# Performance work log

Hardware: AMD Instinct MI355X
Metric: run time of the kernel (lower is better)

Reference implementation:

```python
import jax, jax.numpy as jnp
import numpy as np

B, N, D = 4, 2048, 1024
DF = 4 * D
EPS = 1e-5


def _layernorm(x, w, b):
    mu = jnp.mean(x, axis=-1, keepdims=True)
    var = jnp.mean(jnp.square(x - mu), axis=-1, keepdims=True)
    return (x - mu) * jax.lax.rsqrt(var + EPS) * w + b


def setup_inputs() -> dict:
    key = jax.random.key(0)
    ks = jax.random.split(key, 8)
    x = jax.random.normal(ks[0], (B, N, D), dtype=jnp.float32)
    # conv filter param (torch init is zeros; use small randn for numeric coverage)
    weights = jax.random.normal(ks[1], (1, 1, N), dtype=jnp.float32) * 0.02
    # registered buffer: sqrt(1/(i+1)) per token, shape (1, N, 1)
    scale = jnp.sqrt(1.0 / (jnp.arange(N, dtype=jnp.float32) + 1.0))[None, :, None]
    ln1_w = jnp.ones((D,), jnp.float32)
    ln1_b = jnp.zeros((D,), jnp.float32)
    W1 = jax.random.normal(ks[2], (DF, D), dtype=jnp.float32) * 0.02
    b1 = jnp.zeros((DF,), jnp.float32)
    W2 = jax.random.normal(ks[3], (D, DF), dtype=jnp.float32) * 0.02
    b2 = jnp.zeros((D,), jnp.float32)
    scalar = jax.random.normal(ks[4], (1,), dtype=jnp.float32) * 0.1
    ln2_w = jnp.ones((D,), jnp.float32)
    ln2_b = jnp.zeros((D,), jnp.float32)
    return dict(x=x, weights=weights, scale=scale, ln1_w=ln1_w, ln1_b=ln1_b,
                W1=W1, b1=b1, W2=W2, b2=b2, scalar=scalar, ln2_w=ln2_w, ln2_b=ln2_b)


def reference(x, weights, scale, ln1_w, ln1_b, W1, b1, W2, b2, scalar, ln2_w, ln2_b):
    n = weights.shape[-1]
    # FFT token-mixing conv: operate over token axis. x: (B,N,D) -> (B,D,N)
    xt = jnp.swapaxes(x, -2, -1)
    # real inputs -> rfft/irfft equals real(ifft(fft*fft)) from the torch code
    prod = jnp.fft.rfft(xt, n=2 * n) * jnp.fft.rfft(weights, n=2 * n)
    conv = jnp.fft.irfft(prod, n=2 * n)[..., :n]  # (B,D,N)
    x1 = jnp.swapaxes(conv, -2, -1)               # (B,N,D)
    x1 = _layernorm(x + x1 * scale, ln1_w, ln1_b)
    # GELU MLP (torch F.gelu default = exact erf gelu)
    h = jax.nn.gelu(jnp.einsum('bnd,fd->bnf', x1, W1) + b1, approximate=False)
    mlp = jnp.einsum('bnf,df->bnd', h, W2) + b2
    x2 = _layernorm(x1 + scalar * mlp, ln2_w, ln2_b)
    return x2
```

## Files before the change

kernel.cpp:

```cpp
#include <hip/hip_runtime.h>
#include <cstdint>

typedef float floatx4 __attribute__((ext_vector_type(4)));
typedef float floatx16 __attribute__((ext_vector_type(16)));
typedef int intx8 __attribute__((ext_vector_type(8)));

__device__ __forceinline__ unsigned short f2b(float f) {
  union { float f; unsigned u; } v; v.f = f;
  return (unsigned short)((v.u + 0x7FFFu + ((v.u >> 16) & 1u)) >> 16);
}
__device__ __forceinline__ float b2f(unsigned short h) {
  union { unsigned u; float f; } v; v.u = ((unsigned)h) << 16;
  return v.f;
}

__device__ __forceinline__ void gload_lds16(const void* g, void* l) {
  __builtin_amdgcn_global_load_lds(
      (const __attribute__((address_space(1))) void*)g,
      (__attribute__((address_space(3))) void*)l, 16, 0, 0);
}

__device__ __forceinline__ intx8 lds_read32(const unsigned char* p) {
  union { intx8 v; int4 q[2]; } u;
  u.q[0] = *(const int4*)p;
  u.q[1] = *(const int4*)(p + 16);
  return u.v;
}

__device__ __forceinline__ int swz_scol(int lane) {
  const int q = (lane >> 1) & 3;
  const int r3 = (lane >> 3) & 3;
  const int sbit = lane & 1;
  return ((((q ^ r3) << 1) | sbit) << 4);
}


__global__ void cast_f8x64_kernel(const float* __restrict__ in,
                                  int* __restrict__ out) {
  long i = (long)blockIdx.x * 256 + threadIdx.x;
  float4 v = ((const float4*)in)[i];
  int pk = __builtin_amdgcn_cvt_pk_fp8_f32(v.x * 64.0f, v.y * 64.0f, 0, false);
  pk = __builtin_amdgcn_cvt_pk_fp8_f32(v.z * 64.0f, v.w * 64.0f, pk, true);
  out[i] = pk;
}

__global__ void build_T8_kernel(const float* __restrict__ w,
                                int* __restrict__ T8) {
  long i = (long)blockIdx.x * 256 + threadIdx.x;
  int n = (int)(i >> 9);
  int m0 = (int)(i & 511) * 4;
  float v[4];
#pragma unroll
  for (int r = 0; r < 4; ++r) {
    int m = m0 + r;
    v[r] = (m <= n) ? w[n - m] * 64.0f : 0.0f;
  }
  int pk = __builtin_amdgcn_cvt_pk_fp8_f32(v[0], v[1], 0, false);
  pk = __builtin_amdgcn_cvt_pk_fp8_f32(v[2], v[3], pk, true);
  T8[i] = pk;
}

__global__ void transpose_cast_f8_kernel(const float* __restrict__ x,
                                         unsigned char* __restrict__ xT) {
  __shared__ float tile[32][33];
  int b = blockIdx.z;
  int n0 = blockIdx.y * 32;
  int d0 = blockIdx.x * 32;
  int tx = threadIdx.x;
  int ty = threadIdx.y;
  for (int i = ty; i < 32; i += 8)
    tile[i][tx] = x[((long)b * 2048 + n0 + i) * 1024 + d0 + tx];
  __syncthreads();
  float a = tile[ty * 4 + 0][tx];
  float c = tile[ty * 4 + 1][tx];
  float e = tile[ty * 4 + 2][tx];
  float f = tile[ty * 4 + 3][tx];
  int pk = __builtin_amdgcn_cvt_pk_fp8_f32(a, c, 0, false);
  pk = __builtin_amdgcn_cvt_pk_fp8_f32(e, f, pk, true);
  *(int*)(xT + ((long)b * 1024 + d0 + tx) * 2048 + n0 + ty * 4) = pk;
}

template <int EPI, int NT, bool TRI>
__global__ __launch_bounds__(256, 4) void gemm_f8(
    const unsigned char* __restrict__ A, const unsigned char* __restrict__ B,
    int Kstride, int Kloop, long zsA, long zsB, long zsC,
    int rx, int ryb, int gxn, unsigned sclA, unsigned sclB,
    const float* __restrict__ resid, const float* __restrict__ scale,
    const float* __restrict__ bias,
    float* __restrict__ Cf, unsigned short* __restrict__ Cb,
    unsigned char* __restrict__ C8) {
  __shared__ __align__(16) unsigned char As[16 * 1040];
  __shared__ __align__(16) unsigned char Bs[16 * 1040];
  const int tid = threadIdx.x;
  const int wid = tid >> 6;
  const int lane = tid & 63;
  const int l32 = lane & 31;
  const int half = lane >> 5;
  const int wm = (wid >> 1) * 64;
  const int wn = (wid & 1) * 64;

  const int bid = blockIdx.x;
  const int xcd = bid & 7;
  const int ib = bid >> 3;
  const int ci = ib % rx;
  const int ri = ib / rx;
  long bm, bn;
  if (TRI) {
    bm = (long)(ri == 0 ? xcd : 15 - xcd) * 128;
    bn = (long)ci * 128;
  } else {
    const int gx = xcd % gxn;
    const int gy = xcd / gxn;
    bm = (long)(gy * ryb + ri) * 128;
    bn = (long)(gx * rx + ci) * 128;
  }
  const int bz = blockIdx.z;
  const unsigned char* Ab = A + zsA * bz;
  const unsigned char* Bb = B + zsB * bz;

  floatx16 acc[2][2];
#pragma unroll
  for (int i = 0; i < 2; ++i)
#pragma unroll
    for (int j = 0; j < 2; ++j)
#pragma unroll
      for (int e = 0; e < 16; ++e) acc[i][j][e] = 0.0f;

  const int srow = tid >> 3;
  const int scol = swz_scol(lane);
  const unsigned char* gA[4];
  const unsigned char* gB[4];
  unsigned char* lA[4];
  unsigned char* lB[4];
#pragma unroll
  for (int p = 0; p < 4; ++p) {
    gA[p] = Ab + (bm + p * 32 + srow) * (long)Kstride + scol;
    gB[p] = Bb + (bn + p * 32 + srow) * (long)Kstride + scol;
    lA[p] = As + (p * 4 + wid) * 1040;
    lB[p] = Bs + (p * 4 + wid) * 1040;
  }

  int offA[2][2], offB[2][2];
#pragma unroll
  for (int i = 0; i < 2; ++i)
#pragma unroll
    for (int s = 0; s < 2; ++s) {
      const int ra = wm + i * 32 + l32;
      const int ca = (s * 2 + half) ^ (ra & 3);
      offA[i][s] = (ra >> 3) * 1040 + (ra & 7) * 128 + (ca << 5);
      const int rb = wn + i * 32 + l32;
      const int cb = (s * 2 + half) ^ (rb & 3);
      offB[i][s] = (rb >> 3) * 1040 + (rb & 7) * 128 + (cb << 5);
    }

  const int kend = TRI ? min(Kloop, (int)bm + 128) : Kloop;
  for (int kk = 0; kk < kend; kk += 128) {
    __syncthreads();
#pragma unroll
    for (int p = 0; p < 4; ++p) {
      gload_lds16(gA[p] + kk, lA[p]);
      gload_lds16(gB[p] + kk, lB[p]);
    }
    __syncthreads();
#pragma unroll
    for (int s = 0; s < 2; ++s) {
      intx8 b0 = lds_read32(Bs + offB[0][s]);
      intx8 b1 = lds_read32(Bs + offB[1][s]);
      intx8 a0 = lds_read32(As + offA[0][s]);
      intx8 a1 = lds_read32(As + offA[1][s]);
      acc[0][0] = __builtin_amdgcn_mfma_scale_f32_32x32x64_f8f6f4(
          a0, b0, acc[0][0], 0, 0, 0, sclA, 0, sclB);
      acc[0][1] = __builtin_amdgcn_mfma_scale_f32_32x32x64_f8f6f4(
          a0, b1, acc[0][1], 0, 0, 0, sclA, 0, sclB);
      acc[1][0] = __builtin_amdgcn_mfma_scale_f32_32x32x64_f8f6f4(
          a1, b0, acc[1][0], 0, 0, 0, sclA, 0, sclB);
      acc[1][1] = __builtin_amdgcn_mfma_scale_f32_32x32x64_f8f6f4(
          a1, b1, acc[1][1], 0, 0, 0, sclA, 0, sclB);
    }
  }

#pragma unroll
  for (int i = 0; i < 2; ++i)
#pragma unroll
    for (int j = 0; j < 2; ++j)
#pragma unroll
      for (int r = 0; r < 16; ++r) {
        long row = bm + wm + i * 32 + (r & 3) + 8 * (r >> 2) + 4 * half;
        long col = bn + wn + j * 32 + l32;
        long idx = (long)bz * zsC + row * (long)NT + col;
        float v = acc[i][j][r];
        if (EPI == 0) {
          Cb[idx] = f2b(v);
        } else if (EPI == 1) {
          Cf[idx] = resid[idx] + scale[row] * v;
        } else {
          v += bias[col];
          float u = v * (0.7978845608f + 0.0356774081f * v * v);
          float u2 = u * u;
          float t = __fdividef(u * (15.0f + u2), 15.0f + 6.0f * u2);
          t = fminf(fmaxf(t, -1.0f), 1.0f);
          float g = 0.5f * v * (1.0f + t);
          int pk = __builtin_amdgcn_cvt_pk_fp8_f32(g, 0.0f, 0, false);
          C8[idx] = (unsigned char)(pk & 0xFF);
        }
      }
}

__global__ __launch_bounds__(256) void ln_kernel(
    const float* __restrict__ in, const float* __restrict__ w,
    const float* __restrict__ b, unsigned short* __restrict__ outb,
    int* __restrict__ outf8) {
  const long row = blockIdx.x;
  const int tid = threadIdx.x;
  float4 v = ((const float4*)in)[row * 256 + tid];
  float s = v.x + v.y + v.z + v.w;
  float ss = v.x * v.x + v.y * v.y + v.z * v.z + v.w * v.w;
#pragma unroll
  for (int off = 32; off > 0; off >>= 1) {
    s += __shfl_down(s, off);
    ss += __shfl_down(ss, off);
  }
  __shared__ float red[8];
  const int wid = tid >> 6, lane = tid & 63;
  if (lane == 0) { red[wid] = s; red[4 + wid] = ss; }
  __syncthreads();
  s = red[0] + red[1] + red[2] + red[3];
  ss = red[4] + red[5] + red[6] + red[7];
  const float mu = s * (1.0f / 1024.0f);
  const float var = ss * (1.0f / 1024.0f) - mu * mu;
  const float rs = rsqrtf(var + 1e-5f);
  float4 wv = ((const float4*)w)[tid];
  float4 bv = ((const float4*)b)[tid];
  float o0 = (v.x - mu) * rs * wv.x + bv.x;
  float o1 = (v.y - mu) * rs * wv.y + bv.y;
  float o2 = (v.z - mu) * rs * wv.z + bv.z;
  float o3 = (v.w - mu) * rs * wv.w + bv.w;
  ushort4 u{f2b(o0), f2b(o1), f2b(o2), f2b(o3)};
  ((ushort4*)outb)[row * 256 + tid] = u;
  int pk = __builtin_amdgcn_cvt_pk_fp8_f32(o0, o1, 0, false);
  pk = __builtin_amdgcn_cvt_pk_fp8_f32(o2, o3, pk, true);
  outf8[row * 256 + tid] = pk;
}

__global__ __launch_bounds__(256) void ln2_fused_kernel(
    const unsigned short* __restrict__ y0, const unsigned short* __restrict__ y1,
    const unsigned short* __restrict__ x1b, const float* __restrict__ b2,
    const float* __restrict__ scalar_p, const float* __restrict__ w,
    const float* __restrict__ b, float* __restrict__ out) {
  const long row = blockIdx.x;
  const int tid = threadIdx.x;
  ushort4 a4 = ((const ushort4*)y0)[row * 256 + tid];
  ushort4 c4 = ((const ushort4*)y1)[row * 256 + tid];
  ushort4 xr = ((const ushort4*)x1b)[row * 256 + tid];
  float4 bias = ((const float4*)b2)[tid];
  const float scl = scalar_p[0];
  float4 v;
  v.x = b2f(xr.x) + scl * (b2f(a4.x) + b2f(c4.x) + bias.x);
  v.y = b2f(xr.y) + scl * (b2f(a4.y) + b2f(c4.y) + bias.y);
  v.z = b2f(xr.z) + scl * (b2f(a4.z) + b2f(c4.z) + bias.z);
  v.w = b2f(xr.w) + scl * (b2f(a4.w) + b2f(c4.w) + bias.w);
  float s = v.x + v.y + v.z + v.w;
  float ss = v.x * v.x + v.y * v.y + v.z * v.z + v.w * v.w;
#pragma unroll
  for (int off = 32; off > 0; off >>= 1) {
    s += __shfl_down(s, off);
    ss += __shfl_down(ss, off);
  }
  __shared__ float red[8];
  const int wid = tid >> 6, lane = tid & 63;
  if (lane == 0) { red[wid] = s; red[4 + wid] = ss; }
  __syncthreads();
  s = red[0] + red[1] + red[2] + red[3];
  ss = red[4] + red[5] + red[6] + red[7];
  const float mu = s * (1.0f / 1024.0f);
  const float var = ss * (1.0f / 1024.0f) - mu * mu;
  const float rs = rsqrtf(var + 1e-5f);
  float4 wv = ((const float4*)w)[tid];
  float4 bv = ((const float4*)b)[tid];
  float4 o;
  o.x = (v.x - mu) * rs * wv.x + bv.x;
  o.y = (v.y - mu) * rs * wv.y + bv.y;
  o.z = (v.z - mu) * rs * wv.z + bv.z;
  o.w = (v.w - mu) * rs * wv.w + bv.w;
  ((float4*)out)[row * 256 + tid] = o;
}

extern "C" void kernel_launch(void* const* d_in, const int* in_sizes, int n_in,
                              void* d_out, int out_size, void* d_ws, size_t ws_size,
                              hipStream_t stream) {
  const float* x      = (const float*)d_in[0];
  const float* wconv  = (const float*)d_in[1];
  const float* scale  = (const float*)d_in[2];
  const float* ln1w   = (const float*)d_in[3];
  const float* ln1b   = (const float*)d_in[4];
  const float* W1     = (const float*)d_in[5];
  const float* b1     = (const float*)d_in[6];
  const float* W2     = (const float*)d_in[7];
  const float* b2     = (const float*)d_in[8];
  const float* scalar = (const float*)d_in[9];
  const float* ln2w   = (const float*)d_in[10];
  const float* ln2b   = (const float*)d_in[11];
  float* out = (float*)d_out;

  const unsigned SCL_1  = 0x7F7F7F7Fu;
  const unsigned SCL_64 = 0x79797979u;

  char* ws = (char*)d_ws;
  unsigned char* xT8   = (unsigned char*)ws;  ws += (size_t)4 * 1024 * 2048;
  unsigned char* T8    = (unsigned char*)ws;  ws += (size_t)2048 * 2048;
  unsigned char* W1f8  = (unsigned char*)ws;  ws += (size_t)4096 * 1024;
  unsigned char* W2f8  = (unsigned char*)ws;  ws += (size_t)4096 * 1024;
  float* y             = (float*)ws;          ws += (size_t)8192 * 1024 * 4;
  unsigned short* yb   = (unsigned short*)ws; ws += (size_t)2 * 8192 * 1024 * 2;
  unsigned short* x1b  = (unsigned short*)ws; ws += (size_t)8192 * 1024 * 2;
  unsigned char* x1f8  = (unsigned char*)ws;  ws += (size_t)8192 * 1024;
  unsigned char* h8    = (unsigned char*)ws;  ws += (size_t)8192 * 4096;

  cast_f8x64_kernel<<<4096, 256, 0, stream>>>(W1, (int*)W1f8);
  cast_f8x64_kernel<<<4096, 256, 0, stream>>>(W2, (int*)W2f8);
  build_T8_kernel<<<4096, 256, 0, stream>>>(wconv, (int*)T8);
  transpose_cast_f8_kernel<<<dim3(32, 64, 4), dim3(32, 8), 0, stream>>>(x, xT8);

  gemm_f8<1, 1024, true><<<dim3(128, 1, 4), 256, 0, stream>>>(
      T8, xT8, 2048, 2048, 0L, (long)1024 * 2048, (long)2048 * 1024,
      8, 0, 0, SCL_64, SCL_1, x, scale, nullptr, y, nullptr, nullptr);
  ln_kernel<<<8192, 256, 0, stream>>>(y, ln1w, ln1b, x1b, (int*)x1f8);
  gemm_f8<2, 4096, false><<<dim3(2048, 1, 1), 256, 0, stream>>>(
      x1f8, W1f8, 1024, 1024, 0L, 0L, 0L,
      16, 16, 2, SCL_1, SCL_64, nullptr, nullptr, b1, nullptr, nullptr, h8);
  gemm_f8<0, 1024, false><<<dim3(512, 1, 2), 256, 0, stream>>>(
      h8, W2f8, 4096, 2048, 2048L, 2048L, (long)8192 * 1024,
      8, 8, 1, SCL_1, SCL_64, nullptr, nullptr, nullptr, nullptr, yb, nullptr);
  ln2_fused_kernel<<<8192, 256, 0, stream>>>(
      yb, yb + (size_t)8192 * 1024, x1b, b2, scalar, ln2w, ln2b, out);
}
```

Before: 298.8 us.

## Split triangular conv GEMM along K, fuse prep kernels, widen LDS swizzle

The four preprocessing kernels (weight casts, Toeplitz build, transpose-cast of x) are merged into one launch. The causal Toeplitz conv GEMM is split in two along K to balance the triangular workload, doubling the grid. Each half writes bf16 partials, and the residual-plus-scale combine moves into a new LN1 kernel that reads both halves. The LDS swizzle is widened from 4 to 8 column groups to reduce bank conflicts, at the cost of extra partial-sum traffic and bf16 rounding of the conv output.

```diff
diff --git a/kernel.cpp b/kernel.cpp
--- a/kernel.cpp
+++ b/kernel.cpp
@@ -20,75 +20,74 @@
       (__attribute__((address_space(3))) void*)l, 16, 0, 0);
 }
 
-__device__ __forceinline__ intx8 lds_read32(const unsigned char* p) {
+__device__ __forceinline__ intx8 lds_read32s(const unsigned char* base,
+                                             int lo, int hi) {
   union { intx8 v; int4 q[2]; } u;
-  u.q[0] = *(const int4*)p;
-  u.q[1] = *(const int4*)(p + 16);
+  u.q[0] = *(const int4*)(base + lo);
+  u.q[1] = *(const int4*)(base + hi);
   return u.v;
 }
 
 __device__ __forceinline__ int swz_scol(int lane) {
-  const int q = (lane >> 1) & 3;
-  const int r3 = (lane >> 3) & 3;
-  const int sbit = lane & 1;
-  return ((((q ^ r3) << 1) | sbit) << 4);
-}
-
-
-__global__ void cast_f8x64_kernel(const float* __restrict__ in,
-                                  int* __restrict__ out) {
-  long i = (long)blockIdx.x * 256 + threadIdx.x;
-  float4 v = ((const float4*)in)[i];
-  int pk = __builtin_amdgcn_cvt_pk_fp8_f32(v.x * 64.0f, v.y * 64.0f, 0, false);
-  pk = __builtin_amdgcn_cvt_pk_fp8_f32(v.z * 64.0f, v.w * 64.0f, pk, true);
-  out[i] = pk;
-}
-
-__global__ void build_T8_kernel(const float* __restrict__ w,
-                                int* __restrict__ T8) {
-  long i = (long)blockIdx.x * 256 + threadIdx.x;
-  int n = (int)(i >> 9);
-  int m0 = (int)(i & 511) * 4;
-  float v[4];
-#pragma unroll
-  for (int r = 0; r < 4; ++r) {
-    int m = m0 + r;
-    v[r] = (m <= n) ? w[n - m] * 64.0f : 0.0f;
-  }
-  int pk = __builtin_amdgcn_cvt_pk_fp8_f32(v[0], v[1], 0, false);
-  pk = __builtin_amdgcn_cvt_pk_fp8_f32(v[2], v[3], pk, true);
-  T8[i] = pk;
-}
-
-__global__ void transpose_cast_f8_kernel(const float* __restrict__ x,
-                                         unsigned char* __restrict__ xT) {
-  __shared__ float tile[32][33];
-  int b = blockIdx.z;
-  int n0 = blockIdx.y * 32;
-  int d0 = blockIdx.x * 32;
-  int tx = threadIdx.x;
-  int ty = threadIdx.y;
-  for (int i = ty; i < 32; i += 8)
-    tile[i][tx] = x[((long)b * 2048 + n0 + i) * 1024 + d0 + tx];
-  __syncthreads();
-  float a = tile[ty * 4 + 0][tx];
-  float c = tile[ty * 4 + 1][tx];
-  float e = tile[ty * 4 + 2][tx];
-  float f = tile[ty * 4 + 3][tx];
-  int pk = __builtin_amdgcn_cvt_pk_fp8_f32(a, c, 0, false);
-  pk = __builtin_amdgcn_cvt_pk_fp8_f32(e, f, pk, true);
-  *(int*)(xT + ((long)b * 1024 + d0 + tx) * 2048 + n0 + ty * 4) = pk;
+  return (((lane & 7) ^ ((lane >> 3) & 7)) << 4);
+}
+
+__global__ __launch_bounds__(256) void prep_kernel(
+    const float* __restrict__ W1, const float* __restrict__ W2,
+    const float* __restrict__ wconv, const float* __restrict__ x,
+    int* __restrict__ W1f8, int* __restrict__ W2f8,
+    int* __restrict__ T8, unsigned char* __restrict__ xT) {
+  const int bid = blockIdx.x;
+  const int tid = threadIdx.x;
+  if (bid < 8192) {
+    const float* in = (bid < 4096) ? W1 : W2;
+    int* out = (bid < 4096) ? W1f8 : W2f8;
+    long i = (long)(bid & 4095) * 256 + tid;
+    float4 v = ((const float4*)in)[i];
+    int pk = __builtin_amdgcn_cvt_pk_fp8_f32(v.x * 64.0f, v.y * 64.0f, 0, false);
+    pk = __builtin_amdgcn_cvt_pk_fp8_f32(v.z * 64.0f, v.w * 64.0f, pk, true);
+    out[i] = pk;
+  } else if (bid < 12288) {
+    long i = (long)(bid - 8192) * 256 + tid;
+    int n = (int)(i >> 9);
+    int m0 = (int)(i & 511) * 4;
+    float v[4];
+#pragma unroll
+    for (int r = 0; r < 4; ++r) {
+      int m = m0 + r;
+      v[r] = (m <= n) ? wconv[n - m] * 64.0f : 0.0f;
+    }
+    int pk = __builtin_amdgcn_cvt_pk_fp8_f32(v[0], v[1], 0, false);
+    pk = __builtin_amdgcn_cvt_pk_fp8_f32(v[2], v[3], pk, true);
+    T8[i] = pk;
+  } else {
+    __shared__ float tile[32][33];
+    const int t = bid - 12288;
+    const int d0 = (t & 31) * 32;
+    const int n0 = ((t >> 5) & 63) * 32;
+    const int b = t >> 11;
+    const int tx = tid & 31;
+    const int ty = tid >> 5;
+    for (int i = ty; i < 32; i += 8)
+      tile[i][tx] = x[((long)b * 2048 + n0 + i) * 1024 + d0 + tx];
+    __syncthreads();
+    float a = tile[ty * 4 + 0][tx];
+    float c = tile[ty * 4 + 1][tx];
+    float e = tile[ty * 4 + 2][tx];
+    float f = tile[ty * 4 + 3][tx];
+    int pk = __builtin_amdgcn_cvt_pk_fp8_f32(a, c, 0, false);
+    pk = __builtin_amdgcn_cvt_pk_fp8_f32(e, f, pk, true);
+    *(int*)(xT + ((long)b * 1024 + d0 + tx) * 2048 + n0 + ty * 4) = pk;
+  }
 }
 
 template <int EPI, int NT, bool TRI>
 __global__ __launch_bounds__(256, 4) void gemm_f8(
     const unsigned char* __restrict__ A, const unsigned char* __restrict__ B,
-    int Kstride, int Kloop, long zsA, long zsB, long zsC,
+    int Kstride, int Kloop, long zsA, long zsB, long zsC, long zsP,
     int rx, int ryb, int gxn, unsigned sclA, unsigned sclB,
-    const float* __restrict__ resid, const float* __restrict__ scale,
     const float* __restrict__ bias,
-    float* __restrict__ Cf, unsigned short* __restrict__ Cb,
-    unsigned char* __restrict__ C8) {
+    unsigned short* __restrict__ Cb, unsigned char* __restrict__ C8) {
   __shared__ __align__(16) unsigned char As[16 * 1040];
   __shared__ __align__(16) unsigned char Bs[16 * 1040];
   const int tid = threadIdx.x;
@@ -102,17 +101,29 @@
   const int bid = blockIdx.x;
   const int xcd = bid & 7;
   const int ib = bid >> 3;
-  const int ci = ib % rx;
-  const int ri = ib / rx;
   long bm, bn;
+  int kstart, kend;
+  long pofs = 0;
   if (TRI) {
+    const int ci = ib & 7;
+    const int ri = (ib >> 3) & 1;
+    const int sp = ib >> 4;
     bm = (long)(ri == 0 ? xcd : 15 - xcd) * 128;
     bn = (long)ci * 128;
+    const int T = (int)(bm >> 7) + 1;
+    const int h = (T + 1) >> 1;
+    kstart = (sp ? h : 0) * 128;
+    kend = (sp ? T : h) * 128;
+    pofs = (long)sp * zsP;
   } else {
+    const int ci = ib % rx;
+    const int ri = ib / rx;
     const int gx = xcd % gxn;
     const int gy = xcd / gxn;
     bm = (long)(gy * ryb + ri) * 128;
     bn = (long)(gx * rx + ci) * 128;
+    kstart = 0;
+    kend = Kloop;
   }
   const int bz = blockIdx.z;
   const unsigned char* Ab = A + zsA * bz;
@@ -140,21 +151,23 @@
     lB[p] = Bs + (p * 4 + wid) * 1040;
   }
 
-  int offA[2][2], offB[2][2];
+  int offA_lo[2][2], offA_hi[2][2], offB_lo[2][2], offB_hi[2][2];
 #pragma unroll
   for (int i = 0; i < 2; ++i)
 #pragma unroll
     for (int s = 0; s < 2; ++s) {
-      const int ra = wm + i * 32 + l32;
-      const int ca = (s * 2 + half) ^ (ra & 3);
-      offA[i][s] = (ra >> 3) * 1040 + (ra & 7) * 128 + (ca << 5);
-      const int rb = wn + i * 32 + l32;
-      const int cb = (s * 2 + half) ^ (rb & 3);
-      offB[i][s] = (rb >> 3) * 1040 + (rb & 7) * 128 + (cb << 5);
+      const int q0 = s * 4 + half * 2;
+      const int ra = (int)wm + i * 32 + l32;
+      const int baseA = (ra >> 3) * 1040 + (ra & 7) * 128;
+      offA_lo[i][s] = baseA + ((q0 ^ (ra & 7)) << 4);
+      offA_hi[i][s] = baseA + (((q0 + 1) ^ (ra & 7)) << 4);
+      const int rb = (int)wn + i * 32 + l32;
+      const int baseB = (rb >> 3) * 1040 + (rb & 7) * 128;
+      offB_lo[i][s] = baseB + ((q0 ^ (rb & 7)) << 4);
+      offB_hi[i][s] = baseB + (((q0 + 1) ^ (rb & 7)) << 4);
     }
 
-  const int kend = TRI ? min(Kloop, (int)bm + 128) : Kloop;
-  for (int kk = 0; kk < kend; kk += 128) {
+  for (int kk = kstart; kk < kend; kk += 128) {
     __syncthreads();
 #pragma unroll
     for (int p = 0; p < 4; ++p) {
@@ -164,10 +177,10 @@
     __syncthreads();
 #pragma unroll
     for (int s = 0; s < 2; ++s) {
-      intx8 b0 = lds_read32(Bs + offB[0][s]);
-      intx8 b1 = lds_read32(Bs + offB[1][s]);
-      intx8 a0 = lds_read32(As + offA[0][s]);
-      intx8 a1 = lds_read32(As + offA[1][s]);
+      intx8 b0 = lds_read32s(Bs, offB_lo[0][s], offB_hi[0][s]);
+      intx8 b1 = lds_read32s(Bs, offB_lo[1][s], offB_hi[1][s]);
+      intx8 a0 = lds_read32s(As, offA_lo[0][s], offA_hi[0][s]);
+      intx8 a1 = lds_read32s(As, offA_lo[1][s], offA_hi[1][s]);
       acc[0][0] = __builtin_amdgcn_mfma_scale_f32_32x32x64_f8f6f4(
           a0, b0, acc[0][0], 0, 0, 0, sclA, 0, sclB);
       acc[0][1] = __builtin_amdgcn_mfma_scale_f32_32x32x64_f8f6f4(
@@ -187,12 +200,10 @@
       for (int r = 0; r < 16; ++r) {
         long row = bm + wm + i * 32 + (r & 3) + 8 * (r >> 2) + 4 * half;
         long col = bn + wn + j * 32 + l32;
-        long idx = (long)bz * zsC + row * (long)NT + col;
+        long idx = pofs + (long)bz * zsC + row * (long)NT + col;
         float v = acc[i][j][r];
         if (EPI == 0) {
           Cb[idx] = f2b(v);
-        } else if (EPI == 1) {
-          Cf[idx] = resid[idx] + scale[row] * v;
         } else {
           v += bias[col];
           float u = v * (0.7978845608f + 0.0356774081f * v * v);
@@ -206,13 +217,22 @@
       }
 }
 
-__global__ __launch_bounds__(256) void ln_kernel(
-    const float* __restrict__ in, const float* __restrict__ w,
-    const float* __restrict__ b, unsigned short* __restrict__ outb,
-    int* __restrict__ outf8) {
+__global__ __launch_bounds__(256) void ln1_kernel(
+    const float* __restrict__ x, const unsigned short* __restrict__ c0,
+    const unsigned short* __restrict__ c1, const float* __restrict__ scale,
+    const float* __restrict__ w, const float* __restrict__ b,
+    unsigned short* __restrict__ outb, int* __restrict__ outf8) {
   const long row = blockIdx.x;
   const int tid = threadIdx.x;
-  float4 v = ((const float4*)in)[row * 256 + tid];
+  float4 xv = ((const float4*)x)[row * 256 + tid];
+  ushort4 a4 = ((const ushort4*)c0)[row * 256 + tid];
+  ushort4 e4 = ((const ushort4*)c1)[row * 256 + tid];
+  const float sc = scale[row & 2047];
+  float4 v;
+  v.x = xv.x + sc * (b2f(a4.x) + b2f(e4.x));
+  v.y = xv.y + sc * (b2f(a4.y) + b2f(e4.y));
+  v.z = xv.z + sc * (b2f(a4.z) + b2f(e4.z));
+  v.w = xv.w + sc * (b2f(a4.w) + b2f(e4.w));
   float s = v.x + v.y + v.z + v.w;
   float ss = v.x * v.x + v.y * v.y + v.z * v.z + v.w * v.w;
 #pragma unroll
@@ -315,22 +335,22 @@
   unsigned short* x1b  = (unsigned short*)ws; ws += (size_t)8192 * 1024 * 2;
   unsigned char* x1f8  = (unsigned char*)ws;  ws += (size_t)8192 * 1024;
   unsigned char* h8    = (unsigned char*)ws;  ws += (size_t)8192 * 4096;
-
-  cast_f8x64_kernel<<<4096, 256, 0, stream>>>(W1, (int*)W1f8);
-  cast_f8x64_kernel<<<4096, 256, 0, stream>>>(W2, (int*)W2f8);
-  build_T8_kernel<<<4096, 256, 0, stream>>>(wconv, (int*)T8);
-  transpose_cast_f8_kernel<<<dim3(32, 64, 4), dim3(32, 8), 0, stream>>>(x, xT8);
-
-  gemm_f8<1, 1024, true><<<dim3(128, 1, 4), 256, 0, stream>>>(
+  (void)y;
+
+  prep_kernel<<<20480, 256, 0, stream>>>(W1, W2, wconv, x,
+                                         (int*)W1f8, (int*)W2f8, (int*)T8, xT8);
+
+  gemm_f8<0, 1024, true><<<dim3(256, 1, 4), 256, 0, stream>>>(
       T8, xT8, 2048, 2048, 0L, (long)1024 * 2048, (long)2048 * 1024,
-      8, 0, 0, SCL_64, SCL_1, x, scale, nullptr, y, nullptr, nullptr);
-  ln_kernel<<<8192, 256, 0, stream>>>(y, ln1w, ln1b, x1b, (int*)x1f8);
+      (long)8192 * 1024, 8, 0, 0, SCL_64, SCL_1, nullptr, yb, nullptr);
+  ln1_kernel<<<8192, 256, 0, stream>>>(
+      x, yb, yb + (size_t)8192 * 1024, scale, ln1w, ln1b, x1b, (int*)x1f8);
   gemm_f8<2, 4096, false><<<dim3(2048, 1, 1), 256, 0, stream>>>(
-      x1f8, W1f8, 1024, 1024, 0L, 0L, 0L,
-      16, 16, 2, SCL_1, SCL_64, nullptr, nullptr, b1, nullptr, nullptr, h8);
+      x1f8, W1f8, 1024, 1024, 0L, 0L, 0L, 0L,
+      16, 16, 2, SCL_1, SCL_64, b1, nullptr, h8);
   gemm_f8<0, 1024, false><<<dim3(512, 1, 2), 256, 0, stream>>>(
-      h8, W2f8, 4096, 2048, 2048L, 2048L, (long)8192 * 1024,
-      8, 8, 1, SCL_1, SCL_64, nullptr, nullptr, nullptr, nullptr, yb, nullptr);
+      h8, W2f8, 4096, 2048, 2048L, 2048L, (long)8192 * 1024, 0L,
+      8, 8, 1, SCL_1, SCL_64, nullptr, yb, nullptr);
   ln2_fused_kernel<<<8192, 256, 0, stream>>>(
       yb, yb + (size_t)8192 * 1024, x1b, b2, scalar, ln2w, ln2b, out);
 }
```

Result: faster. 278.0 us (-6.9%).
